# Performance work log

Hardware: AMD Instinct MI355X
Metric: run time of the kernel (lower is better)

## Reference

```python
import jax, jax.numpy as jnp
import numpy as np

C = 1000      # num_classes
U = 10        # proxies_per_class
D = 512       # feature_dim
B = 4096      # batch
ALPHA = 32.0
DELTA = 0.1


def _l2norm(x, axis=-1):
    return x / jnp.linalg.norm(x, axis=axis, keepdims=True).clip(1e-12)


def setup_inputs() -> dict:
    key = jax.random.key(0)
    k1, k2, k3 = jax.random.split(key, 3)
    features = jax.random.normal(k1, (B, D), dtype=jnp.float32)
    labels = jax.random.randint(k2, (B,), 0, C)
    # proxies are initialized to row-normalized gaussians (as in __init__)
    proxies = _l2norm(jax.random.normal(k3, (C * U, D), dtype=jnp.float32))
    return {"features": features, "labels": labels, "proxies": proxies}


def reference(features, labels, proxies):
    # proxy_class_ids: [C*U], class id of each proxy
    class_ids = jnp.repeat(jnp.arange(C), U)

    x = _l2norm(features)          # [B, D]
    p = _l2norm(proxies)           # [P, D], P = C*U
    sim = x @ p.T                  # [B, P]

    # ---- infer_logits, agg='soft', tau=1 ----
    s = sim.reshape(B, C, U)       # per-class proxy similarities
    w = jax.nn.softmax(s, axis=2)
    logits = jnp.sum(w * s, axis=2)  # [B, C], tau=1 so no extra scaling

    # ---- _compute_proxy_loss (Proxy-Anchor) ----
    sim_t = sim.T                                         # [P, B]
    pos_mask = labels[None, :] == class_ids[:, None]      # [P, B]
    neg_inf = jnp.finfo(jnp.float32).min
    z_pos = jnp.where(pos_mask, -ALPHA * (sim_t - DELTA), neg_inf)
    z_neg = jnp.where(pos_mask, neg_inf, ALPHA * (sim_t + DELTA))
    lse_pos = jax.nn.logsumexp(z_pos, axis=1)             # [P]
    lse_neg = jax.nn.logsumexp(z_neg, axis=1)             # [P]
    pos_term = jax.nn.softplus(lse_pos)
    neg_term = jax.nn.softplus(lse_neg)
    has_pos = pos_mask.any(axis=1)
    pos_loss = jnp.where(has_pos, pos_term, 0.0).sum() / jnp.maximum(
        has_pos.sum(), 1).astype(jnp.float32)
    neg_loss = neg_term.mean()
    proxy_loss = pos_loss + neg_loss

    return logits, proxy_loss
```

## Files before the change

### kernel.cpp

```cpp
#include <hip/hip_runtime.h>
#include <hip/hip_bf16.h>

#define C_CLS   1000
#define U_PX    10
#define D_DIM   512
#define B_BATCH 4096
#define P_PX    (C_CLS * U_PX)
#define ALPHA_F 32.0f
#define DELTA_F 0.1f

#define BM 256
#define BN 80
#define BK 64
#define SIMP 84

#define A_OFF   0
#define B_OFF   32768
#define SMEM_SZ 43008

typedef __attribute__((ext_vector_type(8))) short bf16x8;
typedef __attribute__((ext_vector_type(4))) float f32x4;

typedef __attribute__((address_space(1))) const void gv_t;
typedef __attribute__((address_space(3))) void lv_t;

__device__ __forceinline__ void gload_lds16(const void* g, void* lds) {
    __builtin_amdgcn_global_load_lds((gv_t*)g, (lv_t*)lds, 16, 0, 0);
}

__device__ __forceinline__ unsigned int f2bf(float f) {
    union { float f; unsigned u; } c; c.f = f;
    unsigned u = c.u;
    return (u + 0x7FFF + ((u >> 16) & 1)) >> 16;
}

__global__ __launch_bounds__(256) void norm_rows_kernel(const float* __restrict__ feat,
                                                        const float* __restrict__ prox,
                                                        unsigned int* __restrict__ xout,
                                                        unsigned int* __restrict__ pout) {
    const int wid  = threadIdx.x >> 6;
    const int lane = threadIdx.x & 63;
    int row = blockIdx.x * 4 + wid;
    const float* in;
    unsigned int* out;
    if (row < B_BATCH) { in = feat + (size_t)row * D_DIM;   out = xout + (size_t)row * (D_DIM / 2); }
    else { row -= B_BATCH; in = prox + (size_t)row * D_DIM; out = pout + (size_t)row * (D_DIM / 2); }
    const float4 v0 = reinterpret_cast<const float4*>(in)[lane * 2];
    const float4 v1 = reinterpret_cast<const float4*>(in)[lane * 2 + 1];
    float ss = v0.x*v0.x + v0.y*v0.y + v0.z*v0.z + v0.w*v0.w
             + v1.x*v1.x + v1.y*v1.y + v1.z*v1.z + v1.w*v1.w;
    #pragma unroll
    for (int off = 1; off < 64; off <<= 1) ss += __shfl_xor(ss, off, 64);
    const float inv = 1.0f / fmaxf(sqrtf(ss), 1e-12f);
    uint4 o;
    o.x = f2bf(v0.x * inv) | (f2bf(v0.y * inv) << 16);
    o.y = f2bf(v0.z * inv) | (f2bf(v0.w * inv) << 16);
    o.z = f2bf(v1.x * inv) | (f2bf(v1.y * inv) << 16);
    o.w = f2bf(v1.z * inv) | (f2bf(v1.w * inv) << 16);
    *reinterpret_cast<uint4*>(out + lane * 4) = o;
}

__global__ __launch_bounds__(256, 3) void fused_gemm_kernel(
    const unsigned short* __restrict__ xbf,
    const unsigned short* __restrict__ pbf,
    const int*            __restrict__ labels,
    float*                __restrict__ logits,
    double*               __restrict__ pos_sum,
    double*               __restrict__ neg_sum)
{
    __shared__ __align__(16) char smem[SMEM_SZ];
    __shared__ int lab_lds[BM];

    const int t    = threadIdx.x;
    const int m0   = blockIdx.x * BM;
    const int n0   = blockIdx.y * BN;
    const int wid  = t >> 6;
    const int lane = t & 63;
    const int l15  = lane & 15;
    const int kgrp = lane >> 4;

    if (t < BM) lab_lds[t] = labels[m0 + t];

    const int srow = lane >> 3;
    const int scol = (lane & 7) ^ srow;

    const int koff0 = ((kgrp    ) ^ (l15 & 7)) << 4;
    const int koff1 = ((kgrp + 4) ^ (l15 & 7)) << 4;

    f32x4 acc[4][5];
    #pragma unroll
    for (int m = 0; m < 4; ++m)
        #pragma unroll
        for (int n = 0; n < 5; ++n) acc[m][n] = (f32x4){0.f, 0.f, 0.f, 0.f};

    for (int ks = 0; ks < D_DIM / BK; ++ks) {
        const int kbase = ks * BK;
        #pragma unroll
        for (int c = wid; c < 32; c += 4)
            gload_lds16(xbf + (size_t)(m0 + c * 8 + srow) * D_DIM + kbase + scol * 8,
                        smem + A_OFF + c * 1024);
        for (int c = wid; c < 10; c += 4)
            gload_lds16(pbf + (size_t)(n0 + c * 8 + srow) * D_DIM + kbase + scol * 8,
                        smem + B_OFF + c * 1024);
        __syncthreads();
        #pragma unroll
        for (int kk8 = 0; kk8 < 2; ++kk8) {
            const int koff = kk8 ? koff1 : koff0;
            bf16x8 b[5];
            #pragma unroll
            for (int n = 0; n < 5; ++n)
                b[n] = *reinterpret_cast<const bf16x8*>(smem + B_OFF + (n * 16 + l15) * 128 + koff);
            #pragma unroll
            for (int m = 0; m < 4; ++m) {
                const bf16x8 a = *reinterpret_cast<const bf16x8*>(
                    smem + A_OFF + (wid * 64 + m * 16 + l15) * 128 + koff);
                #pragma unroll
                for (int n = 0; n < 5; ++n)
                    acc[m][n] = __builtin_amdgcn_mfma_f32_16x16x32_bf16(a, b[n], acc[m][n], 0, 0, 0);
            }
        }
        __syncthreads();
    }

    {
        int labv[16];
        #pragma unroll
        for (int m = 0; m < 4; ++m)
            #pragma unroll
            for (int r = 0; r < 4; ++r)
                labv[m * 4 + r] = lab_lds[wid * 64 + m * 16 + kgrp * 4 + r];
        #pragma unroll
        for (int n = 0; n < 5; ++n) {
            const int col = n * 16 + l15;
            const int cls = (n0 + col) / U_PX;
            float pos = 0.f, neg = 0.f;
            #pragma unroll
            for (int m = 0; m < 4; ++m)
                #pragma unroll
                for (int r = 0; r < 4; ++r) {
                    const float s = acc[m][n][r];
                    const bool isp = (labv[m * 4 + r] == cls);
                    const float e = __expf(isp ? (-ALPHA_F * (s - DELTA_F))
                                               : ( ALPHA_F * (s + DELTA_F)));
                    if (isp) pos += e; else neg += e;
                }
            pos += __shfl_xor(pos, 16, 64); pos += __shfl_xor(pos, 32, 64);
            neg += __shfl_xor(neg, 16, 64); neg += __shfl_xor(neg, 32, 64);
            if (lane < 16) {
                atomicAdd(&neg_sum[n0 + col], (double)neg);
                if (pos != 0.f) atomicAdd(&pos_sum[n0 + col], (double)pos);
            }
        }
    }

    float* simw = reinterpret_cast<float*>(smem) + wid * (16 * SIMP);
    #pragma unroll
    for (int m = 0; m < 4; ++m) {
        #pragma unroll
        for (int n = 0; n < 5; ++n)
            #pragma unroll
            for (int r = 0; r < 4; ++r)
                simw[(kgrp * 4 + r) * SIMP + n * 16 + l15] = acc[m][n][r];
        #pragma unroll
        for (int it = 0; it < 2; ++it) {
            const int j   = lane + it * 64;
            const int r   = j >> 3;
            const int c   = j & 7;
            const float* s = simw + r * SIMP + c * U_PX;
            float wsum = 0.f, wssum = 0.f;
            #pragma unroll
            for (int u = 0; u < U_PX; ++u) {
                const float sv = s[u];
                const float e = __expf(sv);
                wsum += e; wssum += e * sv;
            }
            logits[(size_t)(m0 + wid * 64 + m * 16 + r) * C_CLS + (n0 / U_PX + c)] = wssum / wsum;
        }
        __builtin_amdgcn_s_waitcnt(0);
    }
}

__global__ __launch_bounds__(256) void finalize_partial_kernel(
    const double* __restrict__ pos_sum,
    const double* __restrict__ neg_sum,
    double*       __restrict__ accum)
{
    const int p = blockIdx.x * 256 + threadIdx.x;
    double pv = 0.0, nv = 0.0;
    int c = 0;
    if (p < P_PX) {
        nv = log1p(neg_sum[p]);
        const double ps = pos_sum[p];
        if (ps != 0.0) { pv = log1p(ps); c = 1; }
    }
    #pragma unroll
    for (int off = 1; off < 64; off <<= 1) {
        pv += __shfl_xor(pv, off, 64);
        nv += __shfl_xor(nv, off, 64);
        c  += __shfl_xor(c,  off, 64);
    }
    if ((threadIdx.x & 63) == 0) {
        atomicAdd(&accum[0], pv);
        atomicAdd(&accum[1], nv);
        atomicAdd((int*)(accum + 2), c);
    }
}

__global__ void finalize_final_kernel(const double* __restrict__ accum,
                                      float* __restrict__ out_loss) {
    if (threadIdx.x == 0) {
        const int cnt = *(const int*)(accum + 2);
        out_loss[0] = (float)(accum[0] / (double)max(cnt, 1) + accum[1] / (double)P_PX);
    }
}

extern "C" void kernel_launch(void* const* d_in, const int* in_sizes, int n_in,
                              void* d_out, int out_size, void* d_ws, size_t ws_size,
                              hipStream_t stream) {
    const float* features = (const float*)d_in[0];
    const int*   labels   = (const int*)d_in[1];
    const float* proxies  = (const float*)d_in[2];
    float* out = (float*)d_out;

    char* ws = (char*)d_ws;
    unsigned short* xbf = (unsigned short*)ws;
    unsigned short* pbf = (unsigned short*)(ws + (size_t)B_BATCH * D_DIM * 2);
    double* pos_sum = (double*)(ws + (size_t)(B_BATCH + P_PX) * D_DIM * 2);
    double* neg_sum = pos_sum + P_PX;
    double* accum   = neg_sum + P_PX;

    hipMemsetAsync(pos_sum, 0, (2 * P_PX + 3) * sizeof(double), stream);

    norm_rows_kernel<<<(B_BATCH + P_PX) / 4, 256, 0, stream>>>(
        features, proxies, (unsigned int*)xbf, (unsigned int*)pbf);

    fused_gemm_kernel<<<dim3(B_BATCH / BM, P_PX / BN), 256, 0, stream>>>(
        xbf, pbf, labels, out, pos_sum, neg_sum);

    finalize_partial_kernel<<<(P_PX + 255) / 256, 256, 0, stream>>>(pos_sum, neg_sum, accum);
    finalize_final_kernel<<<1, 64, 0, stream>>>(accum, out + (size_t)B_BATCH * C_CLS);
}
```

Baseline: 93.39 us.

## Load A operand directly into registers and remap blocks for XCD locality

Measured after the change: 113.8 us. 21.8% more time.

```diff
diff --git a/kernel.cpp b/kernel.cpp
--- a/kernel.cpp
+++ b/kernel.cpp
@@ -14,9 +14,7 @@
 #define BK 64
 #define SIMP 84
 
-#define A_OFF   0
-#define B_OFF   32768
-#define SMEM_SZ 43008
+#define SMEM_SZ (4 * 16 * SIMP * 4)
 
 typedef __attribute__((ext_vector_type(8))) short bf16x8;
 typedef __attribute__((ext_vector_type(4))) float f32x4;
@@ -72,14 +70,16 @@
     __shared__ int lab_lds[BM];
 
     const int t    = threadIdx.x;
-    const int m0   = blockIdx.x * BM;
-    const int n0   = blockIdx.y * BN;
+    const int bid  = blockIdx.x;
+    const int wg   = (bid & 7) * 250 + (bid >> 3);
+    const int m0   = (wg & 15) * BM;
+    const int n0   = (wg >> 4) * BN;
     const int wid  = t >> 6;
     const int lane = t & 63;
     const int l15  = lane & 15;
     const int kgrp = lane >> 4;
 
-    if (t < BM) lab_lds[t] = labels[m0 + t];
+    lab_lds[t] = labels[m0 + t];
 
     const int srow = lane >> 3;
     const int scol = (lane & 7) ^ srow;
@@ -87,6 +87,8 @@
     const int koff0 = ((kgrp    ) ^ (l15 & 7)) << 4;
     const int koff1 = ((kgrp + 4) ^ (l15 & 7)) << 4;
 
+    const unsigned short* xrow = xbf + (size_t)(m0 + wid * 64 + l15) * D_DIM + kgrp * 8;
+
     f32x4 acc[4][5];
     #pragma unroll
     for (int m = 0; m < 4; ++m)
@@ -94,33 +96,35 @@
         for (int n = 0; n < 5; ++n) acc[m][n] = (f32x4){0.f, 0.f, 0.f, 0.f};
 
     for (int ks = 0; ks < D_DIM / BK; ++ks) {
-        const int kbase = ks * BK;
-        #pragma unroll
-        for (int c = wid; c < 32; c += 4)
-            gload_lds16(xbf + (size_t)(m0 + c * 8 + srow) * D_DIM + kbase + scol * 8,
-                        smem + A_OFF + c * 1024);
+        bf16x8 aR[4][2];
+        {
+            const unsigned short* xp = xrow + ks * BK;
+            #pragma unroll
+            for (int m = 0; m < 4; ++m)
+                #pragma unroll
+                for (int k8 = 0; k8 < 2; ++k8)
+                    aR[m][k8] = *reinterpret_cast<const bf16x8*>(xp + m * 16 * D_DIM + k8 * 32);
+        }
+        __syncthreads();
         for (int c = wid; c < 10; c += 4)
-            gload_lds16(pbf + (size_t)(n0 + c * 8 + srow) * D_DIM + kbase + scol * 8,
-                        smem + B_OFF + c * 1024);
+            gload_lds16(pbf + (size_t)(n0 + c * 8 + srow) * D_DIM + ks * BK + scol * 8,
+                        smem + c * 1024);
         __syncthreads();
         #pragma unroll
-        for (int kk8 = 0; kk8 < 2; ++kk8) {
-            const int koff = kk8 ? koff1 : koff0;
+        for (int k8 = 0; k8 < 2; ++k8) {
+            const int koff = k8 ? koff1 : koff0;
             bf16x8 b[5];
             #pragma unroll
             for (int n = 0; n < 5; ++n)
-                b[n] = *reinterpret_cast<const bf16x8*>(smem + B_OFF + (n * 16 + l15) * 128 + koff);
-            #pragma unroll
-            for (int m = 0; m < 4; ++m) {
-                const bf16x8 a = *reinterpret_cast<const bf16x8*>(
-                    smem + A_OFF + (wid * 64 + m * 16 + l15) * 128 + koff);
+                b[n] = *reinterpret_cast<const bf16x8*>(smem + (n * 16 + l15) * 128 + koff);
+            #pragma unroll
+            for (int m = 0; m < 4; ++m)
                 #pragma unroll
                 for (int n = 0; n < 5; ++n)
-                    acc[m][n] = __builtin_amdgcn_mfma_f32_16x16x32_bf16(a, b[n], acc[m][n], 0, 0, 0);
-            }
-        }
-        __syncthreads();
-    }
+                    acc[m][n] = __builtin_amdgcn_mfma_f32_16x16x32_bf16(aR[m][k8], b[n], acc[m][n], 0, 0, 0);
+        }
+    }
+    __syncthreads();
 
     {
         int labv[16];
@@ -234,7 +238,7 @@
     norm_rows_kernel<<<(B_BATCH + P_PX) / 4, 256, 0, stream>>>(
         features, proxies, (unsigned int*)xbf, (unsigned int*)pbf);
 
-    fused_gemm_kernel<<<dim3(B_BATCH / BM, P_PX / BN), 256, 0, stream>>>(
+    fused_gemm_kernel<<<(B_BATCH / BM) * (P_PX / BN), 256, 0, stream>>>(
         xbf, pbf, labels, out, pos_sum, neg_sum);
 
     finalize_partial_kernel<<<(P_PX + 255) / 256, 256, 0, stream>>>(pos_sum, neg_sum, accum);
```

## Fold memset into norm kernel, merge finalize kernels, raise MFMA priority

Applied to the files above, without the earlier changes.

Result: faster. 87.21 us, median of 4 (-6.6%).

```diff
diff --git a/kernel.cpp b/kernel.cpp
--- a/kernel.cpp
+++ b/kernel.cpp
@@ -18,6 +18,9 @@
 #define B_OFF   32768
 #define SMEM_SZ 43008
 
+#define ZERO_DBL (2 * P_PX + 4)
+#define FIN_BLK  ((P_PX + 255) / 256)
+
 typedef __attribute__((ext_vector_type(8))) short bf16x8;
 typedef __attribute__((ext_vector_type(4))) float f32x4;
 
@@ -37,7 +40,11 @@
 __global__ __launch_bounds__(256) void norm_rows_kernel(const float* __restrict__ feat,
                                                         const float* __restrict__ prox,
                                                         unsigned int* __restrict__ xout,
-                                                        unsigned int* __restrict__ pout) {
+                                                        unsigned int* __restrict__ pout,
+                                                        double* __restrict__ zbase) {
+    const int zidx = blockIdx.x * 256 + threadIdx.x;
+    if (zidx < ZERO_DBL) zbase[zidx] = 0.0;
+
     const int wid  = threadIdx.x >> 6;
     const int lane = threadIdx.x & 63;
     int row = blockIdx.x * 4 + wid;
@@ -103,6 +110,7 @@
             gload_lds16(pbf + (size_t)(n0 + c * 8 + srow) * D_DIM + kbase + scol * 8,
                         smem + B_OFF + c * 1024);
         __syncthreads();
+        __builtin_amdgcn_s_setprio(1);
         #pragma unroll
         for (int kk8 = 0; kk8 < 2; ++kk8) {
             const int koff = kk8 ? koff1 : koff0;
@@ -119,6 +127,7 @@
                     acc[m][n] = __builtin_amdgcn_mfma_f32_16x16x32_bf16(a, b[n], acc[m][n], 0, 0, 0);
             }
         }
+        __builtin_amdgcn_s_setprio(0);
         __syncthreads();
     }
 
@@ -180,10 +189,11 @@
     }
 }
 
-__global__ __launch_bounds__(256) void finalize_partial_kernel(
+__global__ __launch_bounds__(256) void finalize_kernel(
     const double* __restrict__ pos_sum,
     const double* __restrict__ neg_sum,
-    double*       __restrict__ accum)
+    double*       __restrict__ accum,
+    float*        __restrict__ out_loss)
 {
     const int p = blockIdx.x * 256 + threadIdx.x;
     double pv = 0.0, nv = 0.0;
@@ -204,13 +214,16 @@
         atomicAdd(&accum[1], nv);
         atomicAdd((int*)(accum + 2), c);
     }
-}
-
-__global__ void finalize_final_kernel(const double* __restrict__ accum,
-                                      float* __restrict__ out_loss) {
+    __syncthreads();
+    __threadfence();
     if (threadIdx.x == 0) {
-        const int cnt = *(const int*)(accum + 2);
-        out_loss[0] = (float)(accum[0] / (double)max(cnt, 1) + accum[1] / (double)P_PX);
+        const unsigned prev = atomicAdd((unsigned*)(accum + 3), 1u);
+        if (prev == FIN_BLK - 1) {
+            const double a0 = atomicAdd(&accum[0], 0.0);
+            const double a1 = atomicAdd(&accum[1], 0.0);
+            const int   cnt = atomicAdd((int*)(accum + 2), 0);
+            out_loss[0] = (float)(a0 / (double)max(cnt, 1) + a1 / (double)P_PX);
+        }
     }
 }
 
@@ -229,14 +242,12 @@
     double* neg_sum = pos_sum + P_PX;
     double* accum   = neg_sum + P_PX;
 
-    hipMemsetAsync(pos_sum, 0, (2 * P_PX + 3) * sizeof(double), stream);
-
     norm_rows_kernel<<<(B_BATCH + P_PX) / 4, 256, 0, stream>>>(
-        features, proxies, (unsigned int*)xbf, (unsigned int*)pbf);
+        features, proxies, (unsigned int*)xbf, (unsigned int*)pbf, pos_sum);
 
     fused_gemm_kernel<<<dim3(B_BATCH / BM, P_PX / BN), 256, 0, stream>>>(
         xbf, pbf, labels, out, pos_sum, neg_sum);
 
-    finalize_partial_kernel<<<(P_PX + 255) / 256, 256, 0, stream>>>(pos_sum, neg_sum, accum);
-    finalize_final_kernel<<<1, 64, 0, stream>>>(accum, out + (size_t)B_BATCH * C_CLS);
-}
+    finalize_kernel<<<FIN_BLK, 256, 0, stream>>>(pos_sum, neg_sum, accum,
+                                                 out + (size_t)B_BATCH * C_CLS);
+}
```
